# Performance work log

Hardware: AMD Instinct MI355X
Metric: run time of the kernel (lower is better)

The kernel has to match this reference:

```python
import jax, jax.numpy as jnp
import numpy as np

TOK_DIM, POS_DIM, HEAD_DIM = 3, 3, 64
D_MODEL, T, B = 128, 4096, 8


def setup_inputs() -> dict:
    key = jax.random.key(0)
    ks = jax.random.split(key, 8)
    s = 0.1
    return {
        "x": jax.random.normal(ks[0], (B, T, TOK_DIM + POS_DIM), jnp.float32),
        "Wq1": jax.random.normal(ks[1], (TOK_DIM, HEAD_DIM), jnp.float32) * s,
        "Wk1": jax.random.normal(ks[2], (TOK_DIM, HEAD_DIM), jnp.float32) * s,
        "Wv1": jax.random.normal(ks[3], (TOK_DIM, HEAD_DIM), jnp.float32) * s,
        "Wq2": jax.random.normal(ks[4], (POS_DIM, HEAD_DIM), jnp.float32) * s,
        "Wk2": jax.random.normal(ks[5], (POS_DIM, HEAD_DIM), jnp.float32) * s,
        "Wv2": jax.random.normal(ks[6], (POS_DIM, HEAD_DIM), jnp.float32) * s,
        "Wout": jax.random.normal(ks[7], (2 * HEAD_DIM, D_MODEL), jnp.float32) * s,
    }


def _attend(q, k, v):
    # q,k,v: [B,T,HEAD_DIM]; causal scaled dot-product attention
    scale = 1.0 / np.sqrt(HEAD_DIM).astype(np.float32)
    scores = jnp.einsum('btd,bsd->bts', q, k) * scale  # [B,T,T]
    t = scores.shape[1]
    causal = jnp.arange(t)[:, None] >= jnp.arange(t)[None, :]
    scores = jnp.where(causal[None], scores, -jnp.inf)
    p = jax.nn.softmax(scores, axis=-1)
    return jnp.einsum('bts,bsd->btd', p, v)


def reference(x, Wq1, Wk1, Wv1, Wq2, Wk2, Wv2, Wout):
    x_tok = x[:, :, :TOK_DIM]
    x_pos = x[:, :, TOK_DIM:]
    out1 = _attend(x_tok @ Wq1, x_tok @ Wk1, x_tok @ Wv1)
    out2 = _attend(x_pos @ Wq2, x_pos @ Wk2, x_pos @ Wv2)
    out = jnp.concatenate([out1, out2], axis=-1)  # [B,T,2*HEAD_DIM]
    return out @ Wout  # [B,T,D_MODEL]
```

## Files before the change

kernel.cpp:

```cpp
#include <hip/hip_runtime.h>
#include <hip/hip_bf16.h>
#include <stdint.h>

#define T_SEQ 4096

typedef float  f32x4   __attribute__((ext_vector_type(4)));
typedef float  f32x16  __attribute__((ext_vector_type(16)));
typedef short  bf16x8  __attribute__((ext_vector_type(8)));
typedef unsigned int u32x4 __attribute__((ext_vector_type(4)));

typedef const __attribute__((address_space(1))) uint32_t* gptr_t;
typedef __attribute__((address_space(3))) uint32_t* lptr_t;

__device__ __forceinline__ uint32_t f2bf1(float f) {
    uint32_t u = __float_as_uint(f);
    return (u + 0x7fffu + ((u >> 16) & 1u)) >> 16;
}
__device__ __forceinline__ short f2bfs(float f) { return (short)f2bf1(f); }
__device__ __forceinline__ uint32_t cvtpk(float lo, float hi) {
    uint32_t r;
    asm("v_cvt_pk_bf16_f32 %0, %1, %2" : "=v"(r) : "v"(lo), "v"(hi));
    return r;
}

__global__ __launch_bounds__(256) void qk_proj(
    const float* __restrict__ x,
    const float* __restrict__ Wq1, const float* __restrict__ Wk1,
    const float* __restrict__ Wq2, const float* __restrict__ Wk2,
    short* __restrict__ Q, short* __restrict__ K)
{
    int idx = blockIdx.x * 256 + threadIdx.x;
    int d = idx & 63;
    int t = (idx >> 6) & (T_SEQ - 1);
    int b = idx >> 18;
    const float* xp = x + (size_t)(b * T_SEQ + t) * 6;
    float x0 = xp[0], x1 = xp[1], x2 = xp[2];
    float x3 = xp[3], x4 = xp[4], x5 = xp[5];
    const float QS = 0.125f * 1.44269504088896340736f;
    float q1 = (x0 * Wq1[d] + x1 * Wq1[64 + d] + x2 * Wq1[128 + d]) * QS;
    float k1 =  x0 * Wk1[d] + x1 * Wk1[64 + d] + x2 * Wk1[128 + d];
    float q2 = (x3 * Wq2[d] + x4 * Wq2[64 + d] + x5 * Wq2[128 + d]) * QS;
    float k2 =  x3 * Wk2[d] + x4 * Wk2[64 + d] + x5 * Wk2[128 + d];
    size_t base1 = ((size_t)(b * 2 + 0) * T_SEQ + t) * 64 + d;
    size_t base2 = ((size_t)(b * 2 + 1) * T_SEQ + t) * 64 + d;
    Q[base1] = f2bfs(q1);  Q[base2] = f2bfs(q2);
    K[base1] = f2bfs(k1);  K[base2] = f2bfs(k2);
}

__global__ __launch_bounds__(256) void v_proj_t(
    const float* __restrict__ x,
    const float* __restrict__ Wv1, const float* __restrict__ Wv2,
    short* __restrict__ Vt)
{
    int bh = blockIdx.x >> 6;
    int tt = blockIdx.x & 63;
    int head = bh & 1, b = bh >> 1;
    int t  = tt * 64 + (threadIdx.x & 63);
    int dg = threadIdx.x >> 6;
    const float* Wv = head ? Wv2 : Wv1;
    const float* xp = x + (size_t)(b * T_SEQ + t) * 6 + head * 3;
    float x0 = xp[0], x1 = xp[1], x2 = xp[2];
    size_t base = (size_t)bh * 64 * T_SEQ + t;
    #pragma unroll
    for (int k = 0; k < 16; ++k) {
        int d = dg * 16 + k;
        float v = x0 * Wv[d] + x1 * Wv[64 + d] + x2 * Wv[128 + d];
        Vt[base + (size_t)d * T_SEQ] = f2bfs(v);
    }
}

__global__ __launch_bounds__(256, 4) void attn(
    const short* __restrict__ Q, const short* __restrict__ K,
    const short* __restrict__ Vt, float* __restrict__ Hf)
{
    __shared__ __align__(16) char smem[32768];

    int id = blockIdx.x;
    int xcd = id & 7, r = id >> 3;
    int bh = xcd * 2 + (r & 1);
    int s  = 63 - (r >> 1);
    int tid = threadIdx.x;
    int W = tid >> 6;
    int lane = tid & 63;
    int ql = lane & 31, h = lane >> 5;
    int tile = W >> 1, half = W & 1;
    int t0 = 64 * s + 32 * tile;
    int q  = t0 + ql;
    int n  = s + 1;
    int head = bh & 1, bb = bh >> 1;

    size_t kvbase = (size_t)bh * (T_SEQ * 64);

    bf16x8 qf[4];
    #pragma unroll
    for (int ks = 0; ks < 4; ++ks)
        qf[ks] = *(const bf16x8*)(Q + kvbase + (size_t)q * 64 + ks * 16 + h * 8);

    int krl = tid >> 3;
    int kcol = ((tid & 7) ^ (krl & 7)) * 8;
    const short* ksrc0 = K + kvbase + kcol;
    const short* vsrc0 = Vt + kvbase + kcol;

    f32x16 acc0, acc1;
    #pragma unroll
    for (int rr = 0; rr < 16; ++rr) { acc0[rr] = 0.f; acc1[rr] = 0.f; }
    float l = 0.f;
    int swz = (ql & 7) << 4;

#define STAGE(bsel, kvv)                                                        \
    {                                                                           \
        char* kb = smem + (bsel) * 16384;                                       \
        char* vb = kb + 8192;                                                   \
        _Pragma("unroll")                                                       \
        for (int z = 0; z < 2; ++z) {                                           \
            int srow = (kvv) + 32 * z + krl;                                    \
            srow = srow > (T_SEQ - 1) ? (T_SEQ - 1) : srow;                     \
            __builtin_amdgcn_global_load_lds(                                   \
                (gptr_t)(ksrc0 + (size_t)srow * 64),                            \
                (lptr_t)(kb + z * 4096 + tid * 16), 16, 0, 0);                  \
        }                                                                       \
        int vkv = (kvv) > (T_SEQ - 64) ? (T_SEQ - 64) : (kvv);                  \
        _Pragma("unroll")                                                       \
        for (int z = 0; z < 2; ++z)                                             \
            __builtin_amdgcn_global_load_lds(                                   \
                (gptr_t)(vsrc0 + (size_t)(32 * z + krl) * T_SEQ + vkv),         \
                (lptr_t)(vb + z * 4096 + tid * 16), 16, 0, 0);                  \
    }

#define QK_SM(pf0, pf1)                                                         \
        {                                                                       \
            f32x16 Sv;                                                          \
            _Pragma("unroll") for (int rr = 0; rr < 16; ++rr) Sv[rr] = 0.f;     \
            Sv = __builtin_amdgcn_mfma_f32_32x32x16_bf16(kf0, qf[0], Sv,0,0,0); \
            Sv = __builtin_amdgcn_mfma_f32_32x32x16_bf16(kf1, qf[1], Sv,0,0,0); \
            Sv = __builtin_amdgcn_mfma_f32_32x32x16_bf16(kf2, qf[2], Sv,0,0,0); \
            Sv = __builtin_amdgcn_mfma_f32_32x32x16_bf16(kf3, qf[3], Sv,0,0,0); \
            bool needmask = (kv0 + 32 * half + 31 > t0);       \
            uint32_t pw[8];                                                     \
            float l0 = 0.f, l1 = 0.f;                                           \
            _Pragma("unroll") for (int e = 0; e < 8; ++e) {                     \
                float p0 = __builtin_amdgcn_exp2f(Sv[2 * e]);                   \
                float p1 = __builtin_amdgcn_exp2f(Sv[2 * e + 1]);               \
                if (needmask) {                                                 \
                    int kv = kv0 + 32 * half + 4 * h + 2 * (e & 1) + 8 * (e >> 1); \
                    p0 = (kv     <= q) ? p0 : 0.f;                              \
                    p1 = (kv + 1 <= q) ? p1 : 0.f;                              \
                }                                                               \
                l0 += p0; l1 += p1;                                             \
                pw[e] = cvtpk(p0, p1);                                          \
            }                                                                   \
            l += l0 + l1;                                                       \
            {                                                                   \
                uint32_t a0 = pw[0], b0 = pw[2], a1 = pw[1], b1 = pw[3];        \
                asm("v_permlane32_swap_b32 %0, %1" : "+v"(a0), "+v"(b0));       \
                asm("v_permlane32_swap_b32 %0, %1" : "+v"(a1), "+v"(b1));       \
                u32x4 fr = {a0, a1, b0, b1};                                    \
                pf0 = __builtin_bit_cast(bf16x8, fr);                           \
                uint32_t c0 = pw[4], d0 = pw[6], c1 = pw[5], d1 = pw[7];        \
                asm("v_permlane32_swap_b32 %0, %1" : "+v"(c0), "+v"(d0));       \
                asm("v_permlane32_swap_b32 %0, %1" : "+v"(c1), "+v"(d1));       \
                u32x4 fr1 = {c0, c1, d0, d1};                                   \
                pf1 = __builtin_bit_cast(bf16x8, fr1);                          \
            }                                                                   \
        }

#define BODY(cc)                                                                \
    {                                                                           \
        const int kv0 = 64 * (cc);                                              \
        if ((cc) + 1 < n) STAGE(((cc) + 1) & 1, kv0 + 64);                      \
        const char* kb = smem + ((cc) & 1) * 16384;                             \
        const char* vb = kb + 8192;                                             \
        const char* krw = kb + (32 * half + ql) * 128;                          \
        bf16x8 kf0 = *(const bf16x8*)(krw + ((0 * 32 + h * 16) ^ swz));         \
        bf16x8 kf1 = *(const bf16x8*)(krw + ((1 * 32 + h * 16) ^ swz));         \
        bf16x8 kf2 = *(const bf16x8*)(krw + ((2 * 32 + h * 16) ^ swz));         \
        bf16x8 kf3 = *(const bf16x8*)(krw + ((3 * 32 + h * 16) ^ swz));         \
        bool act = (kv0 + 32 * half <= t0 + 31);                                \
        bf16x8 pf0, pf1;                                                        \
        __builtin_amdgcn_s_setprio(1);                                          \
        if (act) QK_SM(pf0, pf1)                                                \
        const char* vr0 = vb + ql * 128;                                        \
        const char* vr1 = vb + (32 + ql) * 128;                                 \
        int vc0 = (64 * half + 16 * h) ^ swz;                                   \
        int vc1 = (64 * half + 32 + 16 * h) ^ swz;                              \
        bf16x8 vf00 = *(const bf16x8*)(vr0 + vc0);                              \
        bf16x8 vf01 = *(const bf16x8*)(vr0 + vc1);                              \
        bf16x8 vf10 = *(const bf16x8*)(vr1 + vc0);                              \
        bf16x8 vf11 = *(const bf16x8*)(vr1 + vc1);                              \
        if (act) {                                                              \
            acc0 = __builtin_amdgcn_mfma_f32_32x32x16_bf16(vf00, pf0, acc0, 0, 0, 0); \
            acc0 = __builtin_amdgcn_mfma_f32_32x32x16_bf16(vf01, pf1, acc0, 0, 0, 0); \
            acc1 = __builtin_amdgcn_mfma_f32_32x32x16_bf16(vf10, pf0, acc1, 0, 0, 0); \
            acc1 = __builtin_amdgcn_mfma_f32_32x32x16_bf16(vf11, pf1, acc1, 0, 0, 0); \
        }                                                                       \
        __builtin_amdgcn_s_setprio(0);                                          \
        __syncthreads();                                                        \
    }

    STAGE(0, 0);
    __syncthreads();

    for (int c = 0; c < n; ++c) BODY(c);
#undef BODY
#undef QK_SM
#undef STAGE

    l += __shfl_xor(l, 32);
    float* sg = (float*)smem + tile * 2112 + lane * 33;
    if (half == 1) {
        #pragma unroll
        for (int g = 0; g < 4; ++g) {
            *(f32x4*)(sg + 4 * g)      = f32x4{acc0[4*g+0], acc0[4*g+1], acc0[4*g+2], acc0[4*g+3]};
            *(f32x4*)(sg + 16 + 4 * g) = f32x4{acc1[4*g+0], acc1[4*g+1], acc1[4*g+2], acc1[4*g+3]};
        }
        sg[32] = l;
    }
    __syncthreads();
    if (half == 0) {
        #pragma unroll
        for (int g = 0; g < 4; ++g) {
            f32x4 u0 = *(f32x4*)(sg + 4 * g);
            f32x4 u1 = *(f32x4*)(sg + 16 + 4 * g);
            acc0[4*g+0] += u0[0]; acc0[4*g+1] += u0[1]; acc0[4*g+2] += u0[2]; acc0[4*g+3] += u0[3];
            acc1[4*g+0] += u1[0]; acc1[4*g+1] += u1[1]; acc1[4*g+2] += u1[2]; acc1[4*g+3] += u1[3];
        }
        l += sg[32];
        float rl = 1.0f / l;
        float* hp = Hf + ((size_t)(bb * T_SEQ) + t0 + ql) * 128 + head * 64 + 4 * h;
        #pragma unroll
        for (int g2 = 0; g2 < 4; ++g2) {
            f32x4 s0 = { acc0[g2*4+0]*rl, acc0[g2*4+1]*rl, acc0[g2*4+2]*rl, acc0[g2*4+3]*rl };
            *(f32x4*)(hp + 8 * g2) = s0;
            f32x4 s1 = { acc1[g2*4+0]*rl, acc1[g2*4+1]*rl, acc1[g2*4+2]*rl, acc1[g2*4+3]*rl };
            *(f32x4*)(hp + 32 + 8 * g2) = s1;
        }
    }
}

__global__ __launch_bounds__(256) void prep_wt(
    const float* __restrict__ Wout, short* __restrict__ Wt)
{
    int tid = blockIdx.x * 256 + threadIdx.x;
    int j = tid >> 7, k = tid & 127;
    float v = Wout[k * 128 + j];
    int slot = k >> 3;
    Wt[j * 128 + (((slot ^ (j & 7)) << 3) | (k & 7))] = f2bfs(v);
}

__global__ __launch_bounds__(256) void out_proj(
    const float* Hf, const short* __restrict__ Wt, float* out)
{
    __shared__ __align__(16) char lws[32768];
    int tid = threadIdx.x;
    int w = tid >> 6, lane = tid & 63, c = lane & 15, g = lane >> 4;
    int cs = c & 7;
    #pragma unroll
    for (int z = 0; z < 8; ++z)
        __builtin_amdgcn_global_load_lds((gptr_t)(Wt + z * 2048 + w * 512 + lane * 8),
                                         (lptr_t)(lws + z * 4096 + w * 1024), 16, 0, 0);
    __syncthreads();

    int row0 = blockIdx.x * 64 + w * 16;
    bf16x8 af[4];
    const float* hp = Hf + (size_t)(row0 + c) * 128 + g * 8;
    #pragma unroll
    for (int kc = 0; kc < 4; ++kc) {
        f32x4 x0 = *(const f32x4*)(hp + kc * 32);
        f32x4 x1 = *(const f32x4*)(hp + kc * 32 + 4);
        u32x4 wv = { cvtpk(x0[0], x0[1]), cvtpk(x0[2], x0[3]),
                     cvtpk(x1[0], x1[1]), cvtpk(x1[2], x1[3]) };
        af[kc] = __builtin_bit_cast(bf16x8, wv);
    }
    #pragma unroll
    for (int jt = 0; jt < 8; ++jt) {
        f32x4 accum = {0.f, 0.f, 0.f, 0.f};
        #pragma unroll
        for (int kc = 0; kc < 4; ++kc) {
            int row = jt * 16 + c;
            bf16x8 bfr = *(const bf16x8*)(lws + row * 256 + (((kc * 4 + g) ^ cs) << 4));
            accum = __builtin_amdgcn_mfma_f32_16x16x32_bf16(af[kc], bfr, accum, 0, 0, 0);
        }
        #pragma unroll
        for (int r = 0; r < 4; ++r)
            out[(size_t)(row0 + g * 4 + r) * 128 + jt * 16 + c] = accum[r];
    }
}

extern "C" void kernel_launch(void* const* d_in, const int* in_sizes, int n_in,
                              void* d_out, int out_size, void* d_ws, size_t ws_size,
                              hipStream_t stream)
{
    (void)in_sizes; (void)n_in; (void)out_size; (void)ws_size;
    const float* x    = (const float*)d_in[0];
    const float* Wq1  = (const float*)d_in[1];
    const float* Wk1  = (const float*)d_in[2];
    const float* Wv1  = (const float*)d_in[3];
    const float* Wq2  = (const float*)d_in[4];
    const float* Wk2  = (const float*)d_in[5];
    const float* Wv2  = (const float*)d_in[6];
    const float* Wout = (const float*)d_in[7];
    float* out = (float*)d_out;

    char* ws = (char*)d_ws;
    short* Q  = (short*)(ws);
    short* K  = (short*)(ws + (size_t)8  * 1024 * 1024);
    short* Vt = (short*)(ws + (size_t)16 * 1024 * 1024);
    short* Wt = Q;
    float* Hf = out;

    qk_proj <<<8192, 256, 0, stream>>>(x, Wq1, Wk1, Wq2, Wk2, Q, K);
    v_proj_t<<<1024, 256, 0, stream>>>(x, Wv1, Wv2, Vt);
    attn    <<<1024, 256, 0, stream>>>(Q, K, Vt, Hf);
    prep_wt <<<  64, 256, 0, stream>>>(Wout, Wt);
    out_proj<<< 512, 256, 0, stream>>>(Hf, Wt, out);
}
```

Measured before the change: 96.52 us.

## Split attention KV loop across two blocks and merge partials in out_proj

Doubles the attention grid so that each query tile is handled by two blocks, one taking the even and one the odd KV chunks. Each block writes unnormalized partial outputs and row sums to workspace, and out_proj sums the partials and normalizes before the output projection. This targets load imbalance and low occupancy from the causal triangular work. The cost is extra global traffic for the second partial buffer and the row sums. The reference has no running-max subtraction, so the two partials can be added directly.

```diff
diff --git a/kernel.cpp b/kernel.cpp
--- a/kernel.cpp
+++ b/kernel.cpp
@@ -71,14 +71,17 @@
 
 __global__ __launch_bounds__(256, 4) void attn(
     const short* __restrict__ Q, const short* __restrict__ K,
-    const short* __restrict__ Vt, float* __restrict__ Hf)
+    const short* __restrict__ Vt, float* __restrict__ Hf,
+    float* __restrict__ P1, float* __restrict__ L0, float* __restrict__ L1)
 {
     __shared__ __align__(16) char smem[32768];
 
     int id = blockIdx.x;
-    int xcd = id & 7, r = id >> 3;
-    int bh = xcd * 2 + (r & 1);
-    int s  = 63 - (r >> 1);
+    int xcd = id & 7, rest = id >> 3;
+    int bh = xcd * 2 + (rest & 1);
+    int rem = rest >> 1;
+    int s  = 63 - (rem >> 1);
+    int p  = rem & 1;
     int tid = threadIdx.x;
     int W = tid >> 6;
     int lane = tid & 63;
@@ -87,7 +90,7 @@
     int t0 = 64 * s + 32 * tile;
     int q  = t0 + ql;
     int n  = s + 1;
-    int head = bh & 1, bb = bh >> 1;
+    int nb = (n - p + 1) >> 1;
 
     size_t kvbase = (size_t)bh * (T_SEQ * 64);
 
@@ -112,18 +115,14 @@
         char* kb = smem + (bsel) * 16384;                                       \
         char* vb = kb + 8192;                                                   \
         _Pragma("unroll")                                                       \
-        for (int z = 0; z < 2; ++z) {                                           \
-            int srow = (kvv) + 32 * z + krl;                                    \
-            srow = srow > (T_SEQ - 1) ? (T_SEQ - 1) : srow;                     \
+        for (int z = 0; z < 2; ++z)                                             \
             __builtin_amdgcn_global_load_lds(                                   \
-                (gptr_t)(ksrc0 + (size_t)srow * 64),                            \
+                (gptr_t)(ksrc0 + (size_t)((kvv) + 32 * z + krl) * 64),          \
                 (lptr_t)(kb + z * 4096 + tid * 16), 16, 0, 0);                  \
-        }                                                                       \
-        int vkv = (kvv) > (T_SEQ - 64) ? (T_SEQ - 64) : (kvv);                  \
         _Pragma("unroll")                                                       \
         for (int z = 0; z < 2; ++z)                                             \
             __builtin_amdgcn_global_load_lds(                                   \
-                (gptr_t)(vsrc0 + (size_t)(32 * z + krl) * T_SEQ + vkv),         \
+                (gptr_t)(vsrc0 + (size_t)(32 * z + krl) * T_SEQ + (kvv)),       \
                 (lptr_t)(vb + z * 4096 + tid * 16), 16, 0, 0);                  \
     }
 
@@ -164,11 +163,11 @@
             }                                                                   \
         }
 
-#define BODY(cc)                                                                \
+#define BODY(jj)                                                                \
     {                                                                           \
-        const int kv0 = 64 * (cc);                                              \
-        if ((cc) + 1 < n) STAGE(((cc) + 1) & 1, kv0 + 64);                      \
-        const char* kb = smem + ((cc) & 1) * 16384;                             \
+        const int kv0 = 64 * (p + 2 * (jj));                                    \
+        if ((jj) + 1 < nb) STAGE(((jj) + 1) & 1, kv0 + 128);                    \
+        const char* kb = smem + ((jj) & 1) * 16384;                             \
         const char* vb = kb + 8192;                                             \
         const char* krw = kb + (32 * half + ql) * 128;                          \
         bf16x8 kf0 = *(const bf16x8*)(krw + ((0 * 32 + h * 16) ^ swz));         \
@@ -197,10 +196,10 @@
         __syncthreads();                                                        \
     }
 
-    STAGE(0, 0);
+    if (nb > 0) STAGE(0, 64 * p);
     __syncthreads();
 
-    for (int c = 0; c < n; ++c) BODY(c);
+    for (int j = 0; j < nb; ++j) BODY(j);
 #undef BODY
 #undef QK_SM
 #undef STAGE
@@ -225,15 +224,19 @@
             acc1[4*g+0] += u1[0]; acc1[4*g+1] += u1[1]; acc1[4*g+2] += u1[2]; acc1[4*g+3] += u1[3];
         }
         l += sg[32];
-        float rl = 1.0f / l;
-        float* hp = Hf + ((size_t)(bb * T_SEQ) + t0 + ql) * 128 + head * 64 + 4 * h;
+        int head = bh & 1, bb = bh >> 1;
+        float* Pdst = p ? P1 : Hf;
+        float* Ldst = p ? L1 : L0;
+        float* hp = Pdst + ((size_t)(bb * T_SEQ) + t0 + ql) * 128 + head * 64 + 4 * h;
         #pragma unroll
         for (int g2 = 0; g2 < 4; ++g2) {
-            f32x4 s0 = { acc0[g2*4+0]*rl, acc0[g2*4+1]*rl, acc0[g2*4+2]*rl, acc0[g2*4+3]*rl };
+            f32x4 s0 = { acc0[g2*4+0], acc0[g2*4+1], acc0[g2*4+2], acc0[g2*4+3] };
             *(f32x4*)(hp + 8 * g2) = s0;
-            f32x4 s1 = { acc1[g2*4+0]*rl, acc1[g2*4+1]*rl, acc1[g2*4+2]*rl, acc1[g2*4+3]*rl };
+            f32x4 s1 = { acc1[g2*4+0], acc1[g2*4+1], acc1[g2*4+2], acc1[g2*4+3] };
             *(f32x4*)(hp + 32 + 8 * g2) = s1;
         }
+        if (h == 0)
+            Ldst[(size_t)bh * T_SEQ + t0 + ql] = l;
     }
 }
 
@@ -248,7 +251,9 @@
 }
 
 __global__ __launch_bounds__(256) void out_proj(
-    const float* Hf, const short* __restrict__ Wt, float* out)
+    const float* P0, const float* __restrict__ P1,
+    const float* __restrict__ L0, const float* __restrict__ L1,
+    const short* __restrict__ Wt, float* out)
 {
     __shared__ __align__(16) char lws[32768];
     int tid = threadIdx.x;
@@ -261,14 +266,25 @@
     __syncthreads();
 
     int row0 = blockIdx.x * 64 + w * 16;
+    int r = row0 + c;
+    int b = r >> 12, t = r & (T_SEQ - 1);
+    float rl0 = 1.0f / (L0[(size_t)(b * 2 + 0) * T_SEQ + t] + L1[(size_t)(b * 2 + 0) * T_SEQ + t]);
+    float rl1 = 1.0f / (L0[(size_t)(b * 2 + 1) * T_SEQ + t] + L1[(size_t)(b * 2 + 1) * T_SEQ + t]);
+
     bf16x8 af[4];
-    const float* hp = Hf + (size_t)(row0 + c) * 128 + g * 8;
+    const float* hp0 = P0 + (size_t)r * 128 + g * 8;
+    const float* hp1 = P1 + (size_t)r * 128 + g * 8;
     #pragma unroll
     for (int kc = 0; kc < 4; ++kc) {
-        f32x4 x0 = *(const f32x4*)(hp + kc * 32);
-        f32x4 x1 = *(const f32x4*)(hp + kc * 32 + 4);
-        u32x4 wv = { cvtpk(x0[0], x0[1]), cvtpk(x0[2], x0[3]),
-                     cvtpk(x1[0], x1[1]), cvtpk(x1[2], x1[3]) };
+        float rl = (kc < 2) ? rl0 : rl1;
+        f32x4 x0 = *(const f32x4*)(hp0 + kc * 32);
+        f32x4 x1 = *(const f32x4*)(hp0 + kc * 32 + 4);
+        f32x4 y0 = *(const f32x4*)(hp1 + kc * 32);
+        f32x4 y1 = *(const f32x4*)(hp1 + kc * 32 + 4);
+        u32x4 wv = { cvtpk((x0[0]+y0[0])*rl, (x0[1]+y0[1])*rl),
+                     cvtpk((x0[2]+y0[2])*rl, (x0[3]+y0[3])*rl),
+                     cvtpk((x1[0]+y1[0])*rl, (x1[1]+y1[1])*rl),
+                     cvtpk((x1[2]+y1[2])*rl, (x1[3]+y1[3])*rl) };
         af[kc] = __builtin_bit_cast(bf16x8, wv);
     }
     #pragma unroll
@@ -281,8 +297,8 @@
             accum = __builtin_amdgcn_mfma_f32_16x16x32_bf16(af[kc], bfr, accum, 0, 0, 0);
         }
         #pragma unroll
-        for (int r = 0; r < 4; ++r)
-            out[(size_t)(row0 + g * 4 + r) * 128 + jt * 16 + c] = accum[r];
+        for (int rr = 0; rr < 4; ++rr)
+            out[(size_t)(row0 + g * 4 + rr) * 128 + jt * 16 + c] = accum[rr];
     }
 }
 
@@ -305,12 +321,15 @@
     short* Q  = (short*)(ws);
     short* K  = (short*)(ws + (size_t)8  * 1024 * 1024);
     short* Vt = (short*)(ws + (size_t)16 * 1024 * 1024);
+    float* P1 = (float*)(ws + (size_t)24 * 1024 * 1024);
+    float* L0 = (float*)(ws + (size_t)40 * 1024 * 1024);
+    float* L1 = (float*)(ws + (size_t)40 * 1024 * 1024 + 262144);
     short* Wt = Q;
     float* Hf = out;
 
     qk_proj <<<8192, 256, 0, stream>>>(x, Wq1, Wk1, Wq2, Wk2, Q, K);
     v_proj_t<<<1024, 256, 0, stream>>>(x, Wv1, Wv2, Vt);
-    attn    <<<1024, 256, 0, stream>>>(Q, K, Vt, Hf);
+    attn    <<<2048, 256, 0, stream>>>(Q, K, Vt, Hf, P1, L0, L1);
     prep_wt <<<  64, 256, 0, stream>>>(Wout, Wt);
-    out_proj<<< 512, 256, 0, stream>>>(Hf, Wt, out);
-}
+    out_proj<<< 512, 256, 0, stream>>>(Hf, P1, L0, L1, Wt, out);
+}
```

Measured after the change: 89.08 us. 7.7% less time.
